# Performance work log

Measured on AMD Instinct MI355X. Metric: run time of the kernel, lower is better.

Reference implementation:

```python
import jax, jax.numpy as jnp
import numpy as np

# dims: batch, length, n_values, input_dim, hidden_dim, embed_dim
B, L, V, D_IN, H, E = 8192, 32, 256, 256, 512, 256


def setup_inputs() -> dict:
    key = jax.random.key(0)
    ks = jax.random.split(key, 11)
    s = 0.05  # keep gates/tanh in a reasonable range
    return {
        "x": jax.random.normal(ks[0], (B, D_IN), jnp.float32),
        "emb": jax.random.normal(ks[1], (V, E), jnp.float32) * s,      # nn.Embedding weight
        "sos_embed": jax.random.normal(ks[2], (E,), jnp.float32) * s,
        "W_i2h": jax.random.normal(ks[3], (H, D_IN), jnp.float32) * s,  # input2hidden[0]
        "b_i2h": jax.random.normal(ks[4], (H,), jnp.float32) * s,
        "W_ih": jax.random.normal(ks[5], (3 * H, E), jnp.float32) * s,  # GRU weight_ih_l0 (r,z,n)
        "W_hh": jax.random.normal(ks[6], (3 * H, H), jnp.float32) * s,  # GRU weight_hh_l0
        "b_ih": jax.random.normal(ks[7], (3 * H,), jnp.float32) * s,
        "b_hh": jax.random.normal(ks[8], (3 * H,), jnp.float32) * s,
        "W_out": jax.random.normal(ks[9], (V, H), jnp.float32) * s,     # hidden2output
        "b_out": jax.random.normal(ks[10], (V,), jnp.float32) * s,
    }


def reference(x, emb, sos_embed, W_i2h, b_i2h, W_ih, W_hh, b_ih, b_hh, W_out, b_out):
    # Free-running decode (input=None), eval mode => argmax sampling.
    h0 = x @ W_i2h.T + b_i2h                                   # [B, H] initial hidden
    i0 = jnp.broadcast_to(sos_embed, (x.shape[0], sos_embed.shape[0]))  # [B, E]

    def step(carry, _):
        h, i = carry
        # PyTorch GRU cell: gates ordered (r, z, n)
        gi = i @ W_ih.T + b_ih                                  # [B, 3H]
        gh = h @ W_hh.T + b_hh                                  # [B, 3H]
        ir, iz, i_n = jnp.split(gi, 3, axis=-1)
        hr, hz, h_n = jnp.split(gh, 3, axis=-1)
        r = jax.nn.sigmoid(ir + hr)
        z = jax.nn.sigmoid(iz + hz)
        n = jnp.tanh(i_n + r * h_n)
        h_new = (1.0 - z) * n + z * h                           # [B, H]
        logit = h_new @ W_out.T + b_out                         # [B, V]
        tok = jnp.argmax(logit, axis=-1)                        # [B] int
        return (h_new, emb[tok]), (tok, logit)

    _, (toks, logits) = jax.lax.scan(step, (h0, i0), None, length=L)
    output = toks.T                                             # [B, L]
    logits = jnp.transpose(logits, (1, 0, 2))                   # [B, L, V]
    return output, logits
```

## Files before the change

kernel.cpp:

```cpp
#include <hip/hip_runtime.h>
#include <math.h>

namespace {

constexpr int kB  = 8192;
constexpr int kL  = 32;
constexpr int kV  = 256;
constexpr int kH  = 512;
constexpr int kE  = 256;
constexpr int kH3 = 1536;

__device__ __forceinline__ float sigm(float x) { return 1.0f / (1.0f + expf(-x)); }

__device__ __forceinline__ void gld_lds16(const float* g, float* lds) {
    __builtin_amdgcn_global_load_lds((const __attribute__((address_space(1))) void*)g,
                                     (__attribute__((address_space(3))) void*)lds, 16, 0, 0);
}
__device__ __forceinline__ void gld_lds4(const float* g, float* lds) {
    __builtin_amdgcn_global_load_lds((const __attribute__((address_space(1))) void*)g,
                                     (__attribute__((address_space(3))) void*)lds, 4, 0, 0);
}

__global__ __launch_bounds__(256) void transpose_kernel(
    const float* __restrict__ in, float* __restrict__ out, int R, int C)
{
    __shared__ float tile[32][33];
    const int tx = threadIdx.x & 31, ty = threadIdx.x >> 5;
    const int c0 = blockIdx.x * 32, r0 = blockIdx.y * 32;
#pragma unroll
    for (int i = 0; i < 4; ++i)
        tile[ty + i * 8][tx] = in[(size_t)(r0 + ty + i * 8) * C + c0 + tx];
    __syncthreads();
#pragma unroll
    for (int i = 0; i < 4; ++i)
        out[(size_t)(c0 + ty + i * 8) * R + r0 + tx] = tile[tx][ty + i * 8];
}

__global__ __launch_bounds__(256) void g_table_kernel(
    const float* __restrict__ emb, const float* __restrict__ sos,
    const float* __restrict__ W, const float* __restrict__ bias,
    float* __restrict__ G)
{
    __shared__ __align__(16) float As[32][64];
    __shared__ __align__(16) float Bs[32][64];
    const int tid = threadIdx.x;
    const int tn = tid & 15, tm = tid >> 4;
    const int m0 = blockIdx.x * 64;
    const int n0 = blockIdx.y * 64;
    float acc[4][4] = {};
    for (int kt = 0; kt < 8; ++kt) {
        const int k0 = kt * 32;
#pragma unroll
        for (int i = 0; i < 2; ++i) {
            int l = tid + i * 256;
            int r = l >> 3, kq = l & 7;
            int row = m0 + r;
            float4 v = make_float4(0.f, 0.f, 0.f, 0.f);
            if (row < 256)       v = *(const float4*)(emb + (size_t)row * kE + k0 + kq * 4);
            else if (row == 256) v = *(const float4*)(sos + k0 + kq * 4);
            As[kq*4+0][r] = v.x; As[kq*4+1][r] = v.y; As[kq*4+2][r] = v.z; As[kq*4+3][r] = v.w;
        }
#pragma unroll
        for (int i = 0; i < 2; ++i) {
            int l = tid + i * 256;
            int r = l >> 3, kq = l & 7;
            float4 v = *(const float4*)(W + (size_t)(n0 + r) * kE + k0 + kq * 4);
            Bs[kq*4+0][r] = v.x; Bs[kq*4+1][r] = v.y; Bs[kq*4+2][r] = v.z; Bs[kq*4+3][r] = v.w;
        }
        __syncthreads();
#pragma unroll
        for (int kk = 0; kk < 32; ++kk) {
            const float4 a = *(const float4*)(&As[kk][tm*4]);
            const float4 b = *(const float4*)(&Bs[kk][tn*4]);
            const float av[4] = {a.x, a.y, a.z, a.w};
            const float bv[4] = {b.x, b.y, b.z, b.w};
#pragma unroll
            for (int i = 0; i < 4; ++i)
#pragma unroll
                for (int j = 0; j < 4; ++j)
                    acc[i][j] = fmaf(av[i], bv[j], acc[i][j]);
        }
        __syncthreads();
    }
    const int cb = n0 + tn * 4;
    const float4 bb = *(const float4*)(bias + cb);
    const float bv[4] = {bb.x, bb.y, bb.z, bb.w};
#pragma unroll
    for (int i = 0; i < 4; ++i) {
        int row = m0 + tm * 4 + i;
        if (row < 257) {
            float4 o = make_float4(acc[i][0] + bv[0], acc[i][1] + bv[1],
                                   acc[i][2] + bv[2], acc[i][3] + bv[3]);
            *(float4*)(G + (size_t)row * kH3 + cb) = o;
        }
    }
}

__global__ __launch_bounds__(256) void h0_kernel(
    const float* __restrict__ x, const float* __restrict__ W,
    const float* __restrict__ bias, float* __restrict__ hT)
{
    __shared__ __align__(16) float As[32][64];
    __shared__ __align__(16) float Bs[32][64];
    const int tid = threadIdx.x;
    const int tn = tid & 15, tm = tid >> 4;
    const int m0 = blockIdx.x * 64;
    const int n0 = blockIdx.y * 64;
    float acc[4][4] = {};
    for (int kt = 0; kt < 8; ++kt) {
        const int k0 = kt * 32;
#pragma unroll
        for (int i = 0; i < 2; ++i) {
            int l = tid + i * 256;
            int r = l >> 3, kq = l & 7;
            float4 v = *(const float4*)(x + (size_t)(m0 + r) * kE + k0 + kq * 4);
            As[kq*4+0][r] = v.x; As[kq*4+1][r] = v.y; As[kq*4+2][r] = v.z; As[kq*4+3][r] = v.w;
        }
#pragma unroll
        for (int i = 0; i < 2; ++i) {
            int l = tid + i * 256;
            int r = l >> 3, kq = l & 7;
            float4 v = *(const float4*)(W + (size_t)(n0 + r) * kE + k0 + kq * 4);
            Bs[kq*4+0][r] = v.x; Bs[kq*4+1][r] = v.y; Bs[kq*4+2][r] = v.z; Bs[kq*4+3][r] = v.w;
        }
        __syncthreads();
#pragma unroll
        for (int kk = 0; kk < 32; ++kk) {
            const float4 a = *(const float4*)(&As[kk][tm*4]);
            const float4 b = *(const float4*)(&Bs[kk][tn*4]);
            const float av[4] = {a.x, a.y, a.z, a.w};
            const float bv[4] = {b.x, b.y, b.z, b.w};
#pragma unroll
            for (int i = 0; i < 4; ++i)
#pragma unroll
                for (int j = 0; j < 4; ++j)
                    acc[i][j] = fmaf(av[i], bv[j], acc[i][j]);
        }
        __syncthreads();
    }
    const int cb = n0 + tn * 4;
    const float4 bb = *(const float4*)(bias + cb);
    const float bv[4] = {bb.x, bb.y, bb.z, bb.w};
#pragma unroll
    for (int i = 0; i < 4; ++i) {
        int row = m0 + tm * 4 + i;
#pragma unroll
        for (int c = 0; c < 4; ++c)
            hT[(size_t)(cb + c) * kB + row] = acc[i][c] + bv[c];
    }
}

__global__ __launch_bounds__(256, 2) void gru_step_kernel(
    const float* __restrict__ hT_in, const float* __restrict__ W_hhT,
    const float* __restrict__ b_hh, const float* __restrict__ G,
    const int* __restrict__ tok, const int t, float* __restrict__ hT_out)
{
    __shared__ __align__(16) float As[2][16 * 128];
    __shared__ __align__(16) float Bs[2][16 * 192];
    const int tid = threadIdx.x;
    const int tn = tid & 15;
    const int tm = tid >> 4;
    const int b0 = blockIdx.x * 128;
    const int j0 = blockIdx.y * 64;

    float acc[8][3][4] = {};

    auto stage = [&](int kt, int buf) {
        const int k0 = kt * 16;
        float* as = As[buf];
        float* bs = Bs[buf];
#pragma unroll
        for (int i = 0; i < 2; ++i) {
            int l = tid + i * 256;
            int r = l >> 5, c = l & 31;
            gld_lds16(hT_in + (size_t)(k0 + r) * kB + b0 + c * 4, &as[4 * l]);
        }
#pragma unroll
        for (int i = 0; i < 3; ++i) {
            int l = tid + i * 256;
            int r = l / 48, q = l % 48;
            int g = q >> 4, cc = q & 15;
            gld_lds16(W_hhT + (size_t)(k0 + r) * kH3 + g * kH + j0 + cc * 4, &bs[4 * l]);
        }
    };

    stage(0, 0);
#pragma unroll 1
    for (int kt = 0; kt < 32; ++kt) {
        if (kt < 31) {
            stage(kt + 1, (kt + 1) & 1);
            asm volatile("s_waitcnt vmcnt(5)" ::: "memory");
        } else {
            asm volatile("s_waitcnt vmcnt(0)" ::: "memory");
        }
        __builtin_amdgcn_s_barrier();
        __builtin_amdgcn_sched_barrier(0);
        const float* __restrict__ as = As[kt & 1];
        const float* __restrict__ bs = Bs[kt & 1];
#pragma unroll
        for (int kk = 0; kk < 16; ++kk) {
            const float4 a0 = *(const float4*)&as[kk * 128 + tm * 8];
            const float4 a1 = *(const float4*)&as[kk * 128 + tm * 8 + 4];
            const float4 br = *(const float4*)&bs[kk * 192 + tn * 4];
            const float4 bz = *(const float4*)&bs[kk * 192 + 64 + tn * 4];
            const float4 bn = *(const float4*)&bs[kk * 192 + 128 + tn * 4];
            const float av[8]  = {a0.x, a0.y, a0.z, a0.w, a1.x, a1.y, a1.z, a1.w};
            const float brv[4] = {br.x, br.y, br.z, br.w};
            const float bzv[4] = {bz.x, bz.y, bz.z, bz.w};
            const float bnv[4] = {bn.x, bn.y, bn.z, bn.w};
#pragma unroll
            for (int i = 0; i < 8; ++i)
#pragma unroll
                for (int jj = 0; jj < 4; ++jj) {
                    acc[i][0][jj] = fmaf(av[i], brv[jj], acc[i][0][jj]);
                    acc[i][1][jj] = fmaf(av[i], bzv[jj], acc[i][1][jj]);
                    acc[i][2][jj] = fmaf(av[i], bnv[jj], acc[i][2][jj]);
                }
        }
        __builtin_amdgcn_sched_barrier(0);
        __builtin_amdgcn_s_barrier();
        __builtin_amdgcn_sched_barrier(0);
    }

    const int j  = j0 + tn * 4;
    const int bb = b0 + tm * 8;
    const float4 bhr = *(const float4*)&b_hh[j];
    const float4 bhz = *(const float4*)&b_hh[kH + j];
    const float4 bhn = *(const float4*)&b_hh[2 * kH + j];
    const float bhrv[4] = {bhr.x, bhr.y, bhr.z, bhr.w};
    const float bhzv[4] = {bhz.x, bhz.y, bhz.z, bhz.w};
    const float bhnv[4] = {bhn.x, bhn.y, bhn.z, bhn.w};

    float hp[4][8];
#pragma unroll
    for (int jj = 0; jj < 4; ++jj) {
        const float4 p0 = *(const float4*)&hT_in[(size_t)(j + jj) * kB + bb];
        const float4 p1 = *(const float4*)&hT_in[(size_t)(j + jj) * kB + bb + 4];
        hp[jj][0] = p0.x; hp[jj][1] = p0.y; hp[jj][2] = p0.z; hp[jj][3] = p0.w;
        hp[jj][4] = p1.x; hp[jj][5] = p1.y; hp[jj][6] = p1.z; hp[jj][7] = p1.w;
    }

    int rows[8];
    if (t == 0) {
#pragma unroll
        for (int i = 0; i < 8; ++i) rows[i] = 256;
    } else {
        const int4 t0 = *(const int4*)&tok[bb];
        const int4 t1 = *(const int4*)&tok[bb + 4];
        rows[0] = t0.x; rows[1] = t0.y; rows[2] = t0.z; rows[3] = t0.w;
        rows[4] = t1.x; rows[5] = t1.y; rows[6] = t1.z; rows[7] = t1.w;
    }

    float ho[4][8];
#pragma unroll
    for (int i = 0; i < 8; ++i) {
        const float* Gr = G + (size_t)rows[i] * kH3;
        const float4 gr = *(const float4*)&Gr[j];
        const float4 gz = *(const float4*)&Gr[kH + j];
        const float4 gn = *(const float4*)&Gr[2 * kH + j];
        const float grv[4] = {gr.x, gr.y, gr.z, gr.w};
        const float gzv[4] = {gz.x, gz.y, gz.z, gz.w};
        const float gnv[4] = {gn.x, gn.y, gn.z, gn.w};
#pragma unroll
        for (int jj = 0; jj < 4; ++jj) {
            float r = sigm(grv[jj] + acc[i][0][jj] + bhrv[jj]);
            float z = sigm(gzv[jj] + acc[i][1][jj] + bhzv[jj]);
            float n = tanhf(gnv[jj] + r * (acc[i][2][jj] + bhnv[jj]));
            ho[jj][i] = (1.0f - z) * n + z * hp[jj][i];
        }
    }
#pragma unroll
    for (int jj = 0; jj < 4; ++jj) {
        *(float4*)&hT_out[(size_t)(j + jj) * kB + bb]     =
            make_float4(ho[jj][0], ho[jj][1], ho[jj][2], ho[jj][3]);
        *(float4*)&hT_out[(size_t)(j + jj) * kB + bb + 4] =
            make_float4(ho[jj][4], ho[jj][5], ho[jj][6], ho[jj][7]);
    }
}

__global__ __launch_bounds__(512, 2) void logit_kernel(
    const float* __restrict__ hT, const float* __restrict__ W_outT,
    const float* __restrict__ b_out, int* __restrict__ tok,
    float* __restrict__ out_tok, float* __restrict__ out_logits, const int t)
{
    __shared__ __align__(16) float As[2][32 * 32];
    __shared__ __align__(16) float Bs[2][32 * 256];
    const int tid = threadIdx.x;
    const int tn = tid & 31;
    const int tm = tid >> 5;
    const int b0 = blockIdx.x * 32;
    float acc[2][8] = {};

    auto stage = [&](int kt, int buf) {
        const int k0 = kt * 32;
        float* as = As[buf];
        float* bs = Bs[buf];
#pragma unroll
        for (int i = 0; i < 4; ++i) {
            int l = tid + i * 512;
            int r = l >> 6, c = l & 63;
            gld_lds16(W_outT + (size_t)(k0 + r) * kV + c * 4, &bs[4 * l]);
        }
#pragma unroll
        for (int i = 0; i < 2; ++i) {
            int l = tid + i * 512;
            int r = l >> 5, c = l & 31;
            gld_lds4(hT + (size_t)(k0 + r) * kB + b0 + c, &as[l]);
        }
    };

    stage(0, 0);
#pragma unroll 1
    for (int kt = 0; kt < 16; ++kt) {
        if (kt < 15) {
            stage(kt + 1, (kt + 1) & 1);
            asm volatile("s_waitcnt vmcnt(6)" ::: "memory");
        } else {
            asm volatile("s_waitcnt vmcnt(0)" ::: "memory");
        }
        __builtin_amdgcn_s_barrier();
        __builtin_amdgcn_sched_barrier(0);
        const float* __restrict__ as = As[kt & 1];
        const float* __restrict__ bs = Bs[kt & 1];
#pragma unroll 8
        for (int kk = 0; kk < 32; ++kk) {
            const float2 a = *(const float2*)&as[kk * 32 + tm * 2];
#pragma unroll
            for (int m = 0; m < 8; ++m) {
                const float bv = bs[kk * 256 + tn + m * 32];
                acc[0][m] = fmaf(a.x, bv, acc[0][m]);
                acc[1][m] = fmaf(a.y, bv, acc[1][m]);
            }
        }
        __builtin_amdgcn_sched_barrier(0);
        __builtin_amdgcn_s_barrier();
        __builtin_amdgcn_sched_barrier(0);
    }

    float bo[8];
#pragma unroll
    for (int m = 0; m < 8; ++m) bo[m] = b_out[tn + m * 32];
#pragma unroll
    for (int i = 0; i < 2; ++i) {
        const int b = b0 + tm * 2 + i;
        float mx = -INFINITY; int mi = 0;
        float* lp = out_logits + ((size_t)b * kL + t) * kV;
#pragma unroll
        for (int m = 0; m < 8; ++m) {
            const int vi = tn + m * 32;
            const float v = acc[i][m] + bo[m];
            lp[vi] = v;
            if (v > mx) { mx = v; mi = vi; }
        }
#pragma unroll
        for (int s = 16; s >= 1; s >>= 1) {
            float pm = __shfl_xor(mx, s, 64);
            int   pi = __shfl_xor(mi, s, 64);
            if (pm > mx || (pm == mx && pi < mi)) { mx = pm; mi = pi; }
        }
        if (tn == 0) {
            tok[b] = mi;
            out_tok[(size_t)b * kL + t] = (float)mi;
        }
    }
}

}

extern "C" void kernel_launch(void* const* d_in, const int* in_sizes, int n_in,
                              void* d_out, int out_size, void* d_ws, size_t ws_size,
                              hipStream_t stream) {
    const float* x      = (const float*)d_in[0];
    const float* emb    = (const float*)d_in[1];
    const float* sos    = (const float*)d_in[2];
    const float* W_i2h  = (const float*)d_in[3];
    const float* b_i2h  = (const float*)d_in[4];
    const float* W_ih   = (const float*)d_in[5];
    const float* W_hh   = (const float*)d_in[6];
    const float* b_ih   = (const float*)d_in[7];
    const float* b_hh   = (const float*)d_in[8];
    const float* W_out  = (const float*)d_in[9];
    const float* b_out  = (const float*)d_in[10];

    float* out        = (float*)d_out;
    float* out_tok    = out;
    float* out_logits = out + (size_t)kB * kL;

    float* hA     = (float*)d_ws;
    float* hB     = hA + (size_t)kH * kB;
    float* G      = hB + (size_t)kH * kB;
    float* W_hhT  = G + (size_t)257 * kH3;
    float* W_outT = W_hhT + (size_t)kH * kH3;
    int*   tok    = (int*)(W_outT + (size_t)kH * kV);

    transpose_kernel<<<dim3(kH / 32, kH3 / 32), 256, 0, stream>>>(W_hh, W_hhT, kH3, kH);
    transpose_kernel<<<dim3(kH / 32, kV / 32), 256, 0, stream>>>(W_out, W_outT, kV, kH);
    g_table_kernel<<<dim3(5, kH3 / 64), 256, 0, stream>>>(emb, sos, W_ih, b_ih, G);
    h0_kernel<<<dim3(kB / 64, kH / 64), 256, 0, stream>>>(x, W_i2h, b_i2h, hA);

    for (int t = 0; t < kL; ++t) {
        float* hin  = (t & 1) ? hB : hA;
        float* hout = (t & 1) ? hA : hB;
        gru_step_kernel<<<dim3(kB / 128, kH / 64), 256, 0, stream>>>(
            hin, W_hhT, b_hh, G, tok, t, hout);
        logit_kernel<<<dim3(kB / 32), 512, 0, stream>>>(
            hout, W_outT, b_out, tok, out_tok, out_logits, t);
    }
}
```

Baseline: 6.994 ms.

## Triple-buffer GRU step LDS pipeline with one barrier and register prefetch

The GRU step GEMM moves from double to triple buffering in shared memory. Loads for tile kt+2 are issued after the single per-iteration barrier, which removes the second barrier. The inner loop now prefetches the next kk's LDS operands into registers, a software pipeline. The output GEMM also switches to a one-barrier scheme that issues the next stage after the barrier. The cost is more LDS per block (possible occupancy loss at 2 blocks/CU), more registers, and a tighter hazard margin on buffer reuse.

```diff
diff --git a/kernel.cpp b/kernel.cpp
--- a/kernel.cpp
+++ b/kernel.cpp
@@ -155,8 +155,8 @@
     const float* __restrict__ b_hh, const float* __restrict__ G,
     const int* __restrict__ tok, const int t, float* __restrict__ hT_out)
 {
-    __shared__ __align__(16) float As[2][16 * 128];
-    __shared__ __align__(16) float Bs[2][16 * 192];
+    __shared__ __align__(16) float As[3][16 * 128];
+    __shared__ __align__(16) float Bs[3][16 * 192];
     const int tid = threadIdx.x;
     const int tn = tid & 15;
     const int tm = tid >> 4;
@@ -165,10 +165,8 @@
 
     float acc[8][3][4] = {};
 
-    auto stage = [&](int kt, int buf) {
+    auto stage = [&](int kt, float* as, float* bs) {
         const int k0 = kt * 16;
-        float* as = As[buf];
-        float* bs = Bs[buf];
 #pragma unroll
         for (int i = 0; i < 2; ++i) {
             int l = tid + i * 256;
@@ -184,26 +182,41 @@
         }
     };
 
-    stage(0, 0);
+    float *a_cur = As[0], *a_nxt = As[1], *a_fut = As[2];
+    float *b_cur = Bs[0], *b_nxt = Bs[1], *b_fut = Bs[2];
+
+    stage(0, a_cur, b_cur);
+    stage(1, a_nxt, b_nxt);
+
 #pragma unroll 1
     for (int kt = 0; kt < 32; ++kt) {
-        if (kt < 31) {
-            stage(kt + 1, (kt + 1) & 1);
+        if (kt < 30) {
             asm volatile("s_waitcnt vmcnt(5)" ::: "memory");
         } else {
             asm volatile("s_waitcnt vmcnt(0)" ::: "memory");
         }
         __builtin_amdgcn_s_barrier();
         __builtin_amdgcn_sched_barrier(0);
-        const float* __restrict__ as = As[kt & 1];
-        const float* __restrict__ bs = Bs[kt & 1];
+        if (kt < 30) stage(kt + 2, a_fut, b_fut);
+
+        const float* __restrict__ as = a_cur;
+        const float* __restrict__ bs = b_cur;
+
+        float4 a0 = *(const float4*)&as[0 * 128 + tm * 8];
+        float4 a1 = *(const float4*)&as[0 * 128 + tm * 8 + 4];
+        float4 br = *(const float4*)&bs[0 * 192 + tn * 4];
+        float4 bz = *(const float4*)&bs[0 * 192 + 64 + tn * 4];
+        float4 bn = *(const float4*)&bs[0 * 192 + 128 + tn * 4];
 #pragma unroll
         for (int kk = 0; kk < 16; ++kk) {
-            const float4 a0 = *(const float4*)&as[kk * 128 + tm * 8];
-            const float4 a1 = *(const float4*)&as[kk * 128 + tm * 8 + 4];
-            const float4 br = *(const float4*)&bs[kk * 192 + tn * 4];
-            const float4 bz = *(const float4*)&bs[kk * 192 + 64 + tn * 4];
-            const float4 bn = *(const float4*)&bs[kk * 192 + 128 + tn * 4];
+            float4 na0, na1, nbr, nbz, nbn;
+            if (kk < 15) {
+                na0 = *(const float4*)&as[(kk + 1) * 128 + tm * 8];
+                na1 = *(const float4*)&as[(kk + 1) * 128 + tm * 8 + 4];
+                nbr = *(const float4*)&bs[(kk + 1) * 192 + tn * 4];
+                nbz = *(const float4*)&bs[(kk + 1) * 192 + 64 + tn * 4];
+                nbn = *(const float4*)&bs[(kk + 1) * 192 + 128 + tn * 4];
+            }
             const float av[8]  = {a0.x, a0.y, a0.z, a0.w, a1.x, a1.y, a1.z, a1.w};
             const float brv[4] = {br.x, br.y, br.z, br.w};
             const float bzv[4] = {bz.x, bz.y, bz.z, bz.w};
@@ -216,10 +229,13 @@
                     acc[i][1][jj] = fmaf(av[i], bzv[jj], acc[i][1][jj]);
                     acc[i][2][jj] = fmaf(av[i], bnv[jj], acc[i][2][jj]);
                 }
-        }
+            if (kk < 15) { a0 = na0; a1 = na1; br = nbr; bz = nbz; bn = nbn; }
+        }
+        asm volatile("s_waitcnt lgkmcnt(0)" ::: "memory");
         __builtin_amdgcn_sched_barrier(0);
-        __builtin_amdgcn_s_barrier();
-        __builtin_amdgcn_sched_barrier(0);
+
+        float* ta = a_cur; a_cur = a_nxt; a_nxt = a_fut; a_fut = ta;
+        float* tb = b_cur; b_cur = b_nxt; b_nxt = b_fut; b_fut = tb;
     }
 
     const int j  = j0 + tn * 4;
@@ -312,14 +328,10 @@
     stage(0, 0);
 #pragma unroll 1
     for (int kt = 0; kt < 16; ++kt) {
-        if (kt < 15) {
-            stage(kt + 1, (kt + 1) & 1);
-            asm volatile("s_waitcnt vmcnt(6)" ::: "memory");
-        } else {
-            asm volatile("s_waitcnt vmcnt(0)" ::: "memory");
-        }
+        asm volatile("s_waitcnt vmcnt(0)" ::: "memory");
         __builtin_amdgcn_s_barrier();
         __builtin_amdgcn_sched_barrier(0);
+        if (kt < 15) stage(kt + 1, (kt + 1) & 1);
         const float* __restrict__ as = As[kt & 1];
         const float* __restrict__ bs = Bs[kt & 1];
 #pragma unroll 8
@@ -332,8 +344,7 @@
                 acc[1][m] = fmaf(a.y, bv, acc[1][m]);
             }
         }
-        __builtin_amdgcn_sched_barrier(0);
-        __builtin_amdgcn_s_barrier();
+        asm volatile("s_waitcnt lgkmcnt(0)" ::: "memory");
         __builtin_amdgcn_sched_barrier(0);
     }
 
```

After: 7.672 ms. 9.7% more time.
